# Kernel tuning notes

Measured on AMD Instinct MI355X. Metric: run time of the kernel, lower is better.

## Reference

```python
import jax, jax.numpy as jnp
import numpy as np

B, T = 32, 2048            # batch, seq_len
V = 16                     # vocab_size
H = 256                    # hidden_size
NV = V + 2                 # embedding rows (padding_idx=0 + vocab + delimiter)
NO = V + 1                 # head output size


def setup_inputs() -> dict:
    key = jax.random.key(0)
    ks = jax.random.split(key, 8)
    s = 1.0 / np.sqrt(H).astype(np.float32)
    tokens = jax.random.randint(ks[0], (B, T), 0, NV)
    embed = jax.random.normal(ks[1], (NV, H), jnp.float32) * 0.02
    embed = embed.at[0].set(0.0)  # padding_idx=0
    # GRU params (PyTorch layout: gates [r|z|n] stacked on last dim)
    W_ih = jax.random.uniform(ks[2], (H, 3 * H), jnp.float32, -s, s)
    W_hh = jax.random.uniform(ks[3], (H, 3 * H), jnp.float32, -s, s)
    b_ih = jax.random.uniform(ks[4], (3 * H,), jnp.float32, -s, s)
    b_hh = jax.random.uniform(ks[5], (3 * H,), jnp.float32, -s, s)
    W_head = jax.random.uniform(ks[6], (H, NO), jnp.float32, -s, s)
    b_head = jax.random.uniform(ks[7], (NO,), jnp.float32, -s, s)
    return {"tokens": tokens, "embed": embed, "W_ih": W_ih, "W_hh": W_hh,
            "b_ih": b_ih, "b_hh": b_hh, "W_head": W_head, "b_head": b_head}


def _mogru_scan(x, W_ih, W_hh, b_ih, b_hh):
    # x: [B, T, H]. Precompute all input projections in one big GEMM.
    gi = x @ W_ih + b_ih                      # [B, T, 3H]
    gi_t = jnp.swapaxes(gi, 0, 1)             # [T, B, 3H] for scan
    h0 = jnp.zeros((x.shape[0], W_hh.shape[0]), x.dtype)

    def step(h, gi_step):
        gh = h @ W_hh + b_hh                  # [B, 3H]
        i_r, i_z, i_n = jnp.split(gi_step, 3, axis=-1)
        h_r, h_z, h_n = jnp.split(gh, 3, axis=-1)
        r = jax.nn.sigmoid(i_r + h_r)
        z = jax.nn.sigmoid(i_z + h_z)         # beta: retention gate
        n = jnp.tanh(i_n + r * h_n)
        h_new = (1.0 - z) * n + z * h
        return h_new, (h_new, z)

    h_last, (outs, betas) = jax.lax.scan(step, h0, gi_t)
    return jnp.swapaxes(outs, 0, 1), h_last, jnp.swapaxes(betas, 0, 1)


def reference(tokens, embed, W_ih, W_hh, b_ih, b_hh, W_head, b_head):
    x = embed[tokens]                          # [B, T, H] embedding lookup
    output, _, betas = _mogru_scan(x, W_ih, W_hh, b_ih, b_hh)
    logits = output @ W_head + b_head          # [B, T, V+1]
    return logits, betas
```

## Files before the change

kernel.cpp:

```cpp
#include <hip/hip_runtime.h>

#define BB   32
#define TT   2048
#define HH   256
#define G3   768
#define NVOC 18
#define NOUT 17
#define LOGITS_ELEMS ((size_t)BB * TT * NOUT)

typedef _Float16 h2 __attribute__((ext_vector_type(2)));

__device__ __forceinline__ float bf1(unsigned short u){
  union{unsigned int i; float f;} v; v.i = ((unsigned int)u) << 16; return v.f;
}
__device__ __forceinline__ unsigned short f2bf(float f){
  union{float f; unsigned int i;} v; v.f = f;
  unsigned int lsb = (v.i >> 16) & 1u;
  v.i += 0x7fffu + lsb;
  return (unsigned short)(v.i >> 16);
}
__device__ __forceinline__ float bflo(unsigned int u){
  union{unsigned int i; float f;} v; v.i = u << 16; return v.f;
}
__device__ __forceinline__ float bfhi(unsigned int u){
  union{unsigned int i; float f;} v; v.i = u & 0xffff0000u; return v.f;
}

__device__ __forceinline__ float ld1(const float* p, size_t i){ return p[i]; }
__device__ __forceinline__ float ld1(const unsigned short* p, size_t i){ return bf1(p[i]); }

__device__ __forceinline__ bool detect_f32(const void* W_ih_raw){
  const unsigned short* u = (const unsigned short*)W_ih_raw;
  bool big = false;
  #pragma unroll
  for (int i = 0; i < 64; i++){
    float v = bf1(u[i]);
    big |= !(v >= -0.25f && v <= 0.25f);
  }
  return big;
}

#if __has_builtin(__builtin_amdgcn_fdot2)
#define FDOT2(a,b,c) __builtin_amdgcn_fdot2((a),(b),(c),false)
#else
#define FDOT2(a,b,c) ((c) + (float)(a).x*(float)(b).x + (float)(a).y*(float)(b).y)
#endif

template<typename T>
__device__ __forceinline__ void prep_body(const T* W_hh, _Float16* Wp){
  int j = blockIdx.x;
  int e = threadIdx.x;
  int q = j & 1, p = j >> 1;
  int c = e >> 7, i = e & 127;
  float v = ld1(W_hh, (size_t)(128*q + i) * G3 + 2*p + c);
  Wp[(size_t)j * 256 + e] = (_Float16)v;
}

__global__ __launch_bounds__(256) void k_prep(
    const void* __restrict__ W_hh, const void* __restrict__ W_ih,
    _Float16* __restrict__ Wp)
{
  if (detect_f32(W_ih)) prep_body<float>((const float*)W_hh, Wp);
  else                  prep_body<unsigned short>((const unsigned short*)W_hh, Wp);
}

template<typename T>
__device__ __forceinline__ void proj_body(const T* embed, const T* W_ih,
                                          const T* b_ih, const T* b_hh,
                                          float* proj, float* bb){
  __shared__ float s_e[HH];
  int v = blockIdx.x, j = threadIdx.x;
  if (j < HH) s_e[j] = ld1(embed, (size_t)v * HH + j);
  if (v == 0) bb[j] = ld1(b_hh, (size_t)j);
  __syncthreads();
  float acc = ld1(b_ih, (size_t)j);
  #pragma unroll 8
  for (int k = 0; k < HH; k++)
    acc += s_e[k] * ld1(W_ih, (size_t)k * G3 + j);
  proj[(size_t)v * G3 + j] = acc;
}

__global__ __launch_bounds__(768) void k_proj(
    const void* __restrict__ embed, const void* __restrict__ W_ih,
    const void* __restrict__ b_ih, const void* __restrict__ b_hh,
    float* __restrict__ proj, float* __restrict__ bb)
{
  if (detect_f32(W_ih))
    proj_body<float>((const float*)embed, (const float*)W_ih,
                     (const float*)b_ih, (const float*)b_hh, proj, bb);
  else
    proj_body<unsigned short>((const unsigned short*)embed,
                              (const unsigned short*)W_ih,
                              (const unsigned short*)b_ih,
                              (const unsigned short*)b_hh, proj, bb);
}

__global__ __launch_bounds__(768, 1) void k_scan(
    const int*      __restrict__ tokens,
    const _Float16* __restrict__ Wp,
    const float*    __restrict__ bb,
    const void*     __restrict__ W_ih,
    const float*    __restrict__ proj,
    unsigned short* __restrict__ outs,
    void*           __restrict__ d_out_base)
{
  __shared__ float s_proj[NVOC * G3];
  __shared__ __align__(16) h2 s_h[HH / 2];
  __shared__ float s_z[HH];
  __shared__ float s_n[HH];

  const bool f32m = detect_f32(W_ih);
  const int b = blockIdx.x;
  const int j = threadIdx.x;
  const int q16 = (j & 1) * 16;

  for (int i = j; i < NVOC * G3; i += 768) s_proj[i] = proj[i];

  h2 wA[64], wB[64];
  {
    const float4* wp4 = (const float4*)(Wp + (size_t)j * 256);
    #pragma unroll
    for (int i = 0; i < 16; i++){
      float4 v = wp4[i];
      wA[4*i+0] = __builtin_bit_cast(h2, v.x);
      wA[4*i+1] = __builtin_bit_cast(h2, v.y);
      wA[4*i+2] = __builtin_bit_cast(h2, v.z);
      wA[4*i+3] = __builtin_bit_cast(h2, v.w);
    }
    #pragma unroll
    for (int i = 0; i < 16; i++){
      float4 v = wp4[16 + i];
      wB[4*i+0] = __builtin_bit_cast(h2, v.x);
      wB[4*i+1] = __builtin_bit_cast(h2, v.y);
      wB[4*i+2] = __builtin_bit_cast(h2, v.z);
      wB[4*i+3] = __builtin_bit_cast(h2, v.w);
    }
  }
  const float bhh = bb[j];

  if (j < HH/2) { h2 z; z.x = (_Float16)0.f; z.y = (_Float16)0.f; s_h[j] = z; }
  float h_old = 0.f;

  const int* tptr = tokens + (size_t)b * TT;
  int tok = tptr[0];
  unsigned short* orow   = outs + (size_t)b * TT * HH + j;
  unsigned short* brow_b = (unsigned short*)d_out_base + LOGITS_ELEMS
                           + (size_t)b * TT * HH + (j - HH);
  float*          brow_f = (float*)d_out_base + LOGITS_ELEMS
                           + (size_t)b * TT * HH + (j - HH);

  __syncthreads();

  for (int t = 0; t < TT; t++) {
    int tok_next = (t + 1 < TT) ? tptr[t + 1] : 0;
    const float* pj = s_proj + tok * G3;
    float gi  = pj[j];
    float gin = (j < HH) ? pj[2*HH + j] : 0.f;

    float a0 = 0.f, a1 = 0.f, a2 = 0.f, a3 = 0.f;
    const int4* hp = (const int4*)s_h;
    #pragma unroll
    for (int i = 0; i < 16; i++) {
      int4 hv = hp[q16 + i];
      h2 x0 = __builtin_bit_cast(h2, hv.x);
      h2 x1 = __builtin_bit_cast(h2, hv.y);
      h2 x2 = __builtin_bit_cast(h2, hv.z);
      h2 x3 = __builtin_bit_cast(h2, hv.w);
      a0 = FDOT2(wA[4*i+0], x0, a0);
      a1 = FDOT2(wA[4*i+1], x1, a1);
      a0 = FDOT2(wA[4*i+2], x2, a0);
      a1 = FDOT2(wA[4*i+3], x3, a1);
      a2 = FDOT2(wB[4*i+0], x0, a2);
      a3 = FDOT2(wB[4*i+1], x1, a3);
      a2 = FDOT2(wB[4*i+2], x2, a2);
      a3 = FDOT2(wB[4*i+3], x3, a3);
    }
    float accA = a0 + a1;
    float accB = a2 + a3;
    accA += __shfl_xor(accA, 1);
    accB += __shfl_xor(accB, 1);
    float gh = ((j & 1) ? accB : accA) + bhh;

    float r = 0.f;
    if (j >= 2*HH) {
      s_n[j - 2*HH] = gh;
    } else if (j >= HH) {
      float z = 1.f / (1.f + __expf(-(gi + gh)));
      s_z[j - HH] = z;
      if (f32m) brow_f[(size_t)t * HH] = z;
      else      brow_b[(size_t)t * HH] = f2bf(z);
    } else {
      r = 1.f / (1.f + __expf(-(gi + gh)));
    }
    __syncthreads();

    if (j < HH) {
      float z = s_z[j];
      float x = gin + r * s_n[j];
      x = fminf(fmaxf(x, -15.f), 15.f);
      float e = __expf(2.f * x);
      float n = (e - 1.f) / (e + 1.f);
      float hn = (1.f - z) * n + z * h_old;
      h_old = hn;
      ((_Float16*)s_h)[j] = (_Float16)hn;
      orow[(size_t)t * HH] = f2bf(hn);
    }
    __syncthreads();
    tok = tok_next;
  }
}

template<typename T>
__device__ __forceinline__ void stage_head(const T* W_head, const T* b_head,
                                           float* s_w, float* s_b, int tid){
  for (int i = tid; i < NOUT * HH; i += 256) {
    int o = i / HH, k = i - o * HH;
    s_w[i] = ld1(W_head, (size_t)k * NOUT + o);
  }
  if (tid < NOUT) s_b[tid] = ld1(b_head, (size_t)tid);
}

__global__ __launch_bounds__(256) void k_head(
    const unsigned short* __restrict__ outs,
    const void* __restrict__ W_head,
    const void* __restrict__ b_head,
    const void* __restrict__ W_ih,
    void* __restrict__ logits_out)
{
  __shared__ float s_w[NOUT * HH];
  __shared__ float s_b[NOUT];
  const bool f32m = detect_f32(W_ih);
  const int tid = threadIdx.x;

  if (f32m) stage_head<float>((const float*)W_head, (const float*)b_head,
                              s_w, s_b, tid);
  else      stage_head<unsigned short>((const unsigned short*)W_head,
                                       (const unsigned short*)b_head,
                                       s_w, s_b, tid);
  __syncthreads();

  size_t gid = (size_t)blockIdx.x * 256 + tid;
  if (gid >= LOGITS_ELEMS) return;
  int o = (int)(gid % NOUT);
  size_t row = gid / NOUT;

  const uint4* xp = (const uint4*)(outs + row * HH);
  const float* wv = s_w + o * HH;
  float a0 = 0.f, a1 = 0.f, a2 = 0.f, a3 = 0.f;
  #pragma unroll 8
  for (int kk = 0; kk < 32; kk++) {
    uint4 u = xp[kk];
    int kb = kk * 8;
    a0 += bflo(u.x) * wv[kb+0] + bfhi(u.x) * wv[kb+1];
    a1 += bflo(u.y) * wv[kb+2] + bfhi(u.y) * wv[kb+3];
    a2 += bflo(u.z) * wv[kb+4] + bfhi(u.z) * wv[kb+5];
    a3 += bflo(u.w) * wv[kb+6] + bfhi(u.w) * wv[kb+7];
  }
  float val = ((a0 + a1) + (a2 + a3)) + s_b[o];
  if (f32m) ((float*)logits_out)[gid] = val;
  else      ((unsigned short*)logits_out)[gid] = f2bf(val);
}

extern "C" void kernel_launch(void* const* d_in, const int* in_sizes, int n_in,
                              void* d_out, int out_size, void* d_ws, size_t ws_size,
                              hipStream_t stream)
{
  const int* tokens = (const int*)d_in[0];
  const void* embed  = d_in[1];
  const void* W_ih   = d_in[2];
  const void* W_hh   = d_in[3];
  const void* b_ih   = d_in[4];
  const void* b_hh   = d_in[5];
  const void* W_head = d_in[6];
  const void* b_head = d_in[7];

  char* ws = (char*)d_ws;
  float*          proj = (float*)ws;
  float*          bb   = (float*)(ws + 55296);
  _Float16*       Wp   = (_Float16*)(ws + 55296 + 3072);
  unsigned short* outs = (unsigned short*)(ws + 55296 + 3072 + 393216);

  k_prep<<<G3, 256, 0, stream>>>(W_hh, W_ih, Wp);
  k_proj<<<NVOC, G3, 0, stream>>>(embed, W_ih, b_ih, b_hh, proj, bb);
  k_scan<<<BB, G3, 0, stream>>>(tokens, Wp, bb, W_ih, proj, outs, d_out);
  k_head<<<(int)((LOGITS_ELEMS + 255) / 256), 256, 0, stream>>>(
      outs, W_head, b_head, W_ih, d_out);
}
```

Baseline: 2.719 ms.

## Use MFMA for the recurrent h·W_hh product in the GRU scan

Replaces the per-thread fdot2 dot products in the scan kernel with 16x16x32 f16 MFMA instructions. W_hh is repacked into MFMA B-operand layout and held in registers across 8 waves, and h is broadcast as the A operand. The block shrinks from 768 to 512 threads, gate pre-activations are written to shared memory, and the gate math is consolidated onto 256 threads. Only row 0 of each MFMA output is used, so most of the matrix work is wasted. The intent is to shorten the serial per-timestep latency of the recurrence.

After: 3.381 ms. 24.4% more time.

```diff
diff --git a/kernel.cpp b/kernel.cpp
--- a/kernel.cpp
+++ b/kernel.cpp
@@ -8,7 +8,8 @@
 #define NOUT 17
 #define LOGITS_ELEMS ((size_t)BB * TT * NOUT)
 
-typedef _Float16 h2 __attribute__((ext_vector_type(2)));
+typedef _Float16 f16x8 __attribute__((ext_vector_type(8)));
+typedef float    f32x4 __attribute__((ext_vector_type(4)));
 
 __device__ __forceinline__ float bf1(unsigned short u){
   union{unsigned int i; float f;} v; v.i = ((unsigned int)u) << 16; return v.f;
@@ -40,20 +41,19 @@
   return big;
 }
 
-#if __has_builtin(__builtin_amdgcn_fdot2)
-#define FDOT2(a,b,c) __builtin_amdgcn_fdot2((a),(b),(c),false)
-#else
-#define FDOT2(a,b,c) ((c) + (float)(a).x*(float)(b).x + (float)(a).y*(float)(b).y)
-#endif
-
 template<typename T>
 __device__ __forceinline__ void prep_body(const T* W_hh, _Float16* Wp){
-  int j = blockIdx.x;
-  int e = threadIdx.x;
-  int q = j & 1, p = j >> 1;
-  int c = e >> 7, i = e & 127;
-  float v = ld1(W_hh, (size_t)(128*q + i) * G3 + 2*p + c);
-  Wp[(size_t)j * 256 + e] = (_Float16)v;
+  int s  = blockIdx.x * 256 + threadIdx.x;
+  int l  = s & 63;
+  int k0 = (s >> 6) & 7;
+  int t2 = s >> 9;
+  int row0 = 32*k0 + 8*(l >> 4);
+  int col  = 16*t2 + (l & 15);
+  f16x8 v;
+  #pragma unroll
+  for (int i2 = 0; i2 < 8; i2++)
+    v[i2] = (_Float16)ld1(W_hh, (size_t)(row0 + i2) * G3 + col);
+  ((f16x8*)Wp)[s] = v;
 }
 
 __global__ __launch_bounds__(256) void k_prep(
@@ -95,7 +95,7 @@
                               (const unsigned short*)b_hh, proj, bb);
 }
 
-__global__ __launch_bounds__(768, 1) void k_scan(
+__global__ __launch_bounds__(512, 2) void k_scan(
     const int*      __restrict__ tokens,
     const _Float16* __restrict__ Wp,
     const float*    __restrict__ bb,
@@ -105,108 +105,101 @@
     void*           __restrict__ d_out_base)
 {
   __shared__ float s_proj[NVOC * G3];
-  __shared__ __align__(16) h2 s_h[HH / 2];
-  __shared__ float s_z[HH];
-  __shared__ float s_n[HH];
+  __shared__ __align__(16) _Float16 s_h[HH];
+  __shared__ float s_gh[G3];
 
   const bool f32m = detect_f32(W_ih);
   const int b = blockIdx.x;
   const int j = threadIdx.x;
-  const int q16 = (j & 1) * 16;
-
-  for (int i = j; i < NVOC * G3; i += 768) s_proj[i] = proj[i];
-
-  h2 wA[64], wB[64];
+  const int w = j >> 6;
+  const int l = j & 63;
+  const int g = l >> 4;
+  const int c = l & 15;
+
+  for (int i = j; i < NVOC * G3 / 4; i += 512)
+    ((float4*)s_proj)[i] = ((const float4*)proj)[i];
+
+  f16x8 wB[48];
   {
-    const float4* wp4 = (const float4*)(Wp + (size_t)j * 256);
+    const f16x8* wpp = (const f16x8*)Wp + (size_t)w * 48 * 64 + l;
     #pragma unroll
-    for (int i = 0; i < 16; i++){
-      float4 v = wp4[i];
-      wA[4*i+0] = __builtin_bit_cast(h2, v.x);
-      wA[4*i+1] = __builtin_bit_cast(h2, v.y);
-      wA[4*i+2] = __builtin_bit_cast(h2, v.z);
-      wA[4*i+3] = __builtin_bit_cast(h2, v.w);
-    }
-    #pragma unroll
-    for (int i = 0; i < 16; i++){
-      float4 v = wp4[16 + i];
-      wB[4*i+0] = __builtin_bit_cast(h2, v.x);
-      wB[4*i+1] = __builtin_bit_cast(h2, v.y);
-      wB[4*i+2] = __builtin_bit_cast(h2, v.z);
-      wB[4*i+3] = __builtin_bit_cast(h2, v.w);
-    }
-  }
-  const float bhh = bb[j];
-
-  if (j < HH/2) { h2 z; z.x = (_Float16)0.f; z.y = (_Float16)0.f; s_h[j] = z; }
+    for (int i = 0; i < 48; i++) wB[i] = wpp[(size_t)i * 64];
+  }
+  const float bh0 = bb[96*w +  0 + c];
+  const float bh1 = bb[96*w + 16 + c];
+  const float bh2 = bb[96*w + 32 + c];
+  const float bh3 = bb[96*w + 48 + c];
+  const float bh4 = bb[96*w + 64 + c];
+  const float bh5 = bb[96*w + 80 + c];
+
+  if (j < HH) s_h[j] = (_Float16)0.f;
+
   float h_old = 0.f;
-
   const int* tptr = tokens + (size_t)b * TT;
-  int tok = tptr[0];
+  int tok = 0;
   unsigned short* orow   = outs + (size_t)b * TT * HH + j;
   unsigned short* brow_b = (unsigned short*)d_out_base + LOGITS_ELEMS
-                           + (size_t)b * TT * HH + (j - HH);
+                           + (size_t)b * TT * HH + j;
   float*          brow_f = (float*)d_out_base + LOGITS_ELEMS
-                           + (size_t)b * TT * HH + (j - HH);
+                           + (size_t)b * TT * HH + j;
+  if (j < HH) tok = tptr[0];
 
   __syncthreads();
 
+  const f16x8* hp8 = (const f16x8*)s_h;
+
   for (int t = 0; t < TT; t++) {
-    int tok_next = (t + 1 < TT) ? tptr[t + 1] : 0;
-    const float* pj = s_proj + tok * G3;
-    float gi  = pj[j];
-    float gin = (j < HH) ? pj[2*HH + j] : 0.f;
-
-    float a0 = 0.f, a1 = 0.f, a2 = 0.f, a3 = 0.f;
-    const int4* hp = (const int4*)s_h;
+    int tok_next = 0;
+    if (j < HH) tok_next = (t + 1 < TT) ? tptr[t + 1] : 0;
+
+    f32x4 acc0 = {bh0, bh0, bh0, bh0};
+    f32x4 acc1 = {bh1, bh1, bh1, bh1};
+    f32x4 acc2 = {bh2, bh2, bh2, bh2};
+    f32x4 acc3 = {bh3, bh3, bh3, bh3};
+    f32x4 acc4 = {bh4, bh4, bh4, bh4};
+    f32x4 acc5 = {bh5, bh5, bh5, bh5};
+
     #pragma unroll
-    for (int i = 0; i < 16; i++) {
-      int4 hv = hp[q16 + i];
-      h2 x0 = __builtin_bit_cast(h2, hv.x);
-      h2 x1 = __builtin_bit_cast(h2, hv.y);
-      h2 x2 = __builtin_bit_cast(h2, hv.z);
-      h2 x3 = __builtin_bit_cast(h2, hv.w);
-      a0 = FDOT2(wA[4*i+0], x0, a0);
-      a1 = FDOT2(wA[4*i+1], x1, a1);
-      a0 = FDOT2(wA[4*i+2], x2, a0);
-      a1 = FDOT2(wA[4*i+3], x3, a1);
-      a2 = FDOT2(wB[4*i+0], x0, a2);
-      a3 = FDOT2(wB[4*i+1], x1, a3);
-      a2 = FDOT2(wB[4*i+2], x2, a2);
-      a3 = FDOT2(wB[4*i+3], x3, a3);
+    for (int k0 = 0; k0 < 8; k0++) {
+      f16x8 af = hp8[4*k0 + g];
+      acc0 = __builtin_amdgcn_mfma_f32_16x16x32_f16(af, wB[ 0 + k0], acc0, 0, 0, 0);
+      acc1 = __builtin_amdgcn_mfma_f32_16x16x32_f16(af, wB[ 8 + k0], acc1, 0, 0, 0);
+      acc2 = __builtin_amdgcn_mfma_f32_16x16x32_f16(af, wB[16 + k0], acc2, 0, 0, 0);
+      acc3 = __builtin_amdgcn_mfma_f32_16x16x32_f16(af, wB[24 + k0], acc3, 0, 0, 0);
+      acc4 = __builtin_amdgcn_mfma_f32_16x16x32_f16(af, wB[32 + k0], acc4, 0, 0, 0);
+      acc5 = __builtin_amdgcn_mfma_f32_16x16x32_f16(af, wB[40 + k0], acc5, 0, 0, 0);
     }
-    float accA = a0 + a1;
-    float accB = a2 + a3;
-    accA += __shfl_xor(accA, 1);
-    accB += __shfl_xor(accB, 1);
-    float gh = ((j & 1) ? accB : accA) + bhh;
-
-    float r = 0.f;
-    if (j >= 2*HH) {
-      s_n[j - 2*HH] = gh;
-    } else if (j >= HH) {
-      float z = 1.f / (1.f + __expf(-(gi + gh)));
-      s_z[j - HH] = z;
+    {
+      float v1 = (g == 0) ? acc0[0] : (g == 1) ? acc1[0]
+               : (g == 2) ? acc2[0] : acc3[0];
+      s_gh[96*w + l] = v1;
+      if (l < 32) {
+        float v2 = (g == 0) ? acc4[0] : acc5[0];
+        s_gh[96*w + 64 + l] = v2;
+      }
+    }
+    __syncthreads();
+
+    if (j < HH) {
+      const float* pj = s_proj + tok * G3;
+      float ghr = s_gh[j];
+      float ghz = s_gh[HH + j];
+      float ghn = s_gh[2*HH + j];
+      float r = 1.f / (1.f + __expf(-(pj[j] + ghr)));
+      float z = 1.f / (1.f + __expf(-(pj[HH + j] + ghz)));
       if (f32m) brow_f[(size_t)t * HH] = z;
       else      brow_b[(size_t)t * HH] = f2bf(z);
-    } else {
-      r = 1.f / (1.f + __expf(-(gi + gh)));
-    }
-    __syncthreads();
-
-    if (j < HH) {
-      float z = s_z[j];
-      float x = gin + r * s_n[j];
+      float x = pj[2*HH + j] + r * ghn;
       x = fminf(fmaxf(x, -15.f), 15.f);
       float e = __expf(2.f * x);
       float n = (e - 1.f) / (e + 1.f);
       float hn = (1.f - z) * n + z * h_old;
       h_old = hn;
-      ((_Float16*)s_h)[j] = (_Float16)hn;
+      s_h[j] = (_Float16)hn;
       orow[(size_t)t * HH] = f2bf(hn);
+      tok = tok_next;
     }
     __syncthreads();
-    tok = tok_next;
   }
 }
 
@@ -280,9 +273,9 @@
   _Float16*       Wp   = (_Float16*)(ws + 55296 + 3072);
   unsigned short* outs = (unsigned short*)(ws + 55296 + 3072 + 393216);
 
-  k_prep<<<G3, 256, 0, stream>>>(W_hh, W_ih, Wp);
+  k_prep<<<96, 256, 0, stream>>>(W_hh, W_ih, Wp);
   k_proj<<<NVOC, G3, 0, stream>>>(embed, W_ih, b_ih, b_hh, proj, bb);
-  k_scan<<<BB, G3, 0, stream>>>(tokens, Wp, bb, W_ih, proj, outs, d_out);
+  k_scan<<<BB, 512, 0, stream>>>(tokens, Wp, bb, W_ih, proj, outs, d_out);
   k_head<<<(int)((LOGITS_ELEMS + 255) / 256), 256, 0, stream>>>(
       outs, W_head, b_head, W_ih, d_out);
 }
```

## Remap GRU scan to 512 threads computing all gates per hidden unit, one barrier per step

Applied to the files above, without the earlier changes.

The recurrent scan now uses 512 threads, where each pair of threads owns one hidden unit and computes its r, z and n gate dot products together. The gate combination then happens in registers after a DPP pair swap, so the s_z/s_n staging and one of the two per-step barriers are no longer needed. The hidden state is double-buffered in LDS and tokens are staged in shared memory. The intermediate output becomes fp16 so the head kernel can use fdot2 against fp16 weights. The cost is higher register pressure (48 float4 weight registers per thread) and a hand-written barrier asm.

Result: faster. 2.651 ms (-2.5%).

```diff
diff --git a/kernel.cpp b/kernel.cpp
--- a/kernel.cpp
+++ b/kernel.cpp
@@ -19,12 +19,6 @@
   v.i += 0x7fffu + lsb;
   return (unsigned short)(v.i >> 16);
 }
-__device__ __forceinline__ float bflo(unsigned int u){
-  union{unsigned int i; float f;} v; v.i = u << 16; return v.f;
-}
-__device__ __forceinline__ float bfhi(unsigned int u){
-  union{unsigned int i; float f;} v; v.i = u & 0xffff0000u; return v.f;
-}
 
 __device__ __forceinline__ float ld1(const float* p, size_t i){ return p[i]; }
 __device__ __forceinline__ float ld1(const unsigned short* p, size_t i){ return bf1(p[i]); }
@@ -46,22 +40,48 @@
 #define FDOT2(a,b,c) ((c) + (float)(a).x*(float)(b).x + (float)(a).y*(float)(b).y)
 #endif
 
+__device__ __forceinline__ h2 bch2(unsigned int u){ return __builtin_bit_cast(h2, u); }
+__device__ __forceinline__ h2 bch2f(float f){ return __builtin_bit_cast(h2, f); }
+
+__device__ __forceinline__ float pair_swap(float v){
+  int i = __builtin_bit_cast(int, v);
+  i = __builtin_amdgcn_mov_dpp(i, 0xB1, 0xF, 0xF, true);
+  return __builtin_bit_cast(float, i);
+}
+
+__device__ __forceinline__ void bar_lds(){
+  asm volatile("s_waitcnt lgkmcnt(0)\n\ts_barrier" ::: "memory");
+}
+
 template<typename T>
-__device__ __forceinline__ void prep_body(const T* W_hh, _Float16* Wp){
-  int j = blockIdx.x;
-  int e = threadIdx.x;
-  int q = j & 1, p = j >> 1;
-  int c = e >> 7, i = e & 127;
-  float v = ld1(W_hh, (size_t)(128*q + i) * G3 + 2*p + c);
-  Wp[(size_t)j * 256 + e] = (_Float16)v;
+__device__ __forceinline__ void prep_body(const T* W_hh, float4* Wp4){
+  int s   = blockIdx.x * 256 + threadIdx.x;
+  int tid = s & 511;
+  int jg  = s >> 9;
+  int p   = tid >> 1, q = tid & 1;
+  int g   = jg >> 4,  jx = jg & 15;
+  int col = (g << 8) + p;
+  int k0  = (q << 7) + (jx << 3);
+  float c0, c1, c2, c3;
+  #pragma unroll
+  for (int c = 0; c < 4; c++){
+    h2 pr;
+    pr.x = (_Float16)ld1(W_hh, (size_t)(k0 + 2*c    ) * G3 + col);
+    pr.y = (_Float16)ld1(W_hh, (size_t)(k0 + 2*c + 1) * G3 + col);
+    float fc = __builtin_bit_cast(float, pr);
+    if (c == 0) c0 = fc; else if (c == 1) c1 = fc;
+    else if (c == 2) c2 = fc; else c3 = fc;
+  }
+  float4 v; v.x = c0; v.y = c1; v.z = c2; v.w = c3;
+  Wp4[s] = v;
 }
 
 __global__ __launch_bounds__(256) void k_prep(
     const void* __restrict__ W_hh, const void* __restrict__ W_ih,
-    _Float16* __restrict__ Wp)
-{
-  if (detect_f32(W_ih)) prep_body<float>((const float*)W_hh, Wp);
-  else                  prep_body<unsigned short>((const unsigned short*)W_hh, Wp);
+    float4* __restrict__ Wp4)
+{
+  if (detect_f32(W_ih)) prep_body<float>((const float*)W_hh, Wp4);
+  else                  prep_body<unsigned short>((const unsigned short*)W_hh, Wp4);
 }
 
 template<typename T>
@@ -95,139 +115,136 @@
                               (const unsigned short*)b_hh, proj, bb);
 }
 
-__global__ __launch_bounds__(768, 1) void k_scan(
-    const int*      __restrict__ tokens,
-    const _Float16* __restrict__ Wp,
-    const float*    __restrict__ bb,
-    const void*     __restrict__ W_ih,
-    const float*    __restrict__ proj,
-    unsigned short* __restrict__ outs,
-    void*           __restrict__ d_out_base)
+__global__ __launch_bounds__(512, 2) void k_scan(
+    const int*    __restrict__ tokens,
+    const float4* __restrict__ Wp4,
+    const float*  __restrict__ bb,
+    const void*   __restrict__ W_ih,
+    const float*  __restrict__ proj,
+    _Float16*     __restrict__ outs,
+    void*         __restrict__ d_out_base)
 {
   __shared__ float s_proj[NVOC * G3];
-  __shared__ __align__(16) h2 s_h[HH / 2];
-  __shared__ float s_z[HH];
-  __shared__ float s_n[HH];
+  __shared__ int   s_tok[TT];
+  __shared__ __align__(16) _Float16 s_h[2][HH];
 
   const bool f32m = detect_f32(W_ih);
-  const int b = blockIdx.x;
-  const int j = threadIdx.x;
-  const int q16 = (j & 1) * 16;
-
-  for (int i = j; i < NVOC * G3; i += 768) s_proj[i] = proj[i];
-
-  h2 wA[64], wB[64];
+  const int b   = blockIdx.x;
+  const int tid = threadIdx.x;
+  const int p   = tid >> 1;
+  const int q   = tid & 1;
+
+  for (int i = tid; i < NVOC * G3 / 4; i += 512)
+    ((float4*)s_proj)[i] = ((const float4*)proj)[i];
+  ((int4*)s_tok)[tid] = ((const int4*)(tokens + (size_t)b * TT))[tid];
+
+  float4 wreg[48];
   {
-    const float4* wp4 = (const float4*)(Wp + (size_t)j * 256);
+    const float4* wp = Wp4 + tid;
     #pragma unroll
-    for (int i = 0; i < 16; i++){
-      float4 v = wp4[i];
-      wA[4*i+0] = __builtin_bit_cast(h2, v.x);
-      wA[4*i+1] = __builtin_bit_cast(h2, v.y);
-      wA[4*i+2] = __builtin_bit_cast(h2, v.z);
-      wA[4*i+3] = __builtin_bit_cast(h2, v.w);
+    for (int i = 0; i < 48; i++) wreg[i] = wp[(size_t)i * 512];
+  }
+  const float bhr = bb[p];
+  const float bhz = bb[HH + p];
+  const float bhn = bb[2*HH + p];
+
+  if (tid < HH) s_h[0][tid] = (_Float16)0.f;
+  float h_old = 0.f;
+
+  _Float16*       orow   = outs + (size_t)b * TT * HH + p;
+  unsigned short* brow_b = (unsigned short*)d_out_base + LOGITS_ELEMS
+                           + (size_t)b * TT * HH + p;
+  float*          brow_f = (float*)d_out_base + LOGITS_ELEMS
+                           + (size_t)b * TT * HH + p;
+
+  __syncthreads();
+
+  for (int t = 0; t < TT; t++) {
+    int tok = s_tok[t];
+    const float* pj = s_proj + tok * G3;
+    float gir = pj[p];
+    float giz = pj[HH + p];
+    float gin = pj[2*HH + p];
+
+    const int4* hb = (const int4*)(&s_h[t & 1][0]) + (q << 4);
+
+    float r0=0.f,r1=0.f,r2=0.f,r3=0.f;
+    float z0=0.f,z1=0.f,z2=0.f,z3=0.f;
+    float n0=0.f,n1=0.f,n2=0.f,n3=0.f;
+    #pragma unroll
+    for (int jx = 0; jx < 16; jx++) {
+      int4 hv = hb[jx];
+      h2 x0 = bch2((unsigned)hv.x);
+      h2 x1 = bch2((unsigned)hv.y);
+      h2 x2 = bch2((unsigned)hv.z);
+      h2 x3 = bch2((unsigned)hv.w);
+      float4 wr = wreg[jx];
+      float4 wz = wreg[16 + jx];
+      float4 wn = wreg[32 + jx];
+      r0 = FDOT2(bch2f(wr.x), x0, r0);
+      r1 = FDOT2(bch2f(wr.y), x1, r1);
+      r2 = FDOT2(bch2f(wr.z), x2, r2);
+      r3 = FDOT2(bch2f(wr.w), x3, r3);
+      z0 = FDOT2(bch2f(wz.x), x0, z0);
+      z1 = FDOT2(bch2f(wz.y), x1, z1);
+      z2 = FDOT2(bch2f(wz.z), x2, z2);
+      z3 = FDOT2(bch2f(wz.w), x3, z3);
+      n0 = FDOT2(bch2f(wn.x), x0, n0);
+      n1 = FDOT2(bch2f(wn.y), x1, n1);
+      n2 = FDOT2(bch2f(wn.z), x2, n2);
+      n3 = FDOT2(bch2f(wn.w), x3, n3);
     }
-    #pragma unroll
-    for (int i = 0; i < 16; i++){
-      float4 v = wp4[16 + i];
-      wB[4*i+0] = __builtin_bit_cast(h2, v.x);
-      wB[4*i+1] = __builtin_bit_cast(h2, v.y);
-      wB[4*i+2] = __builtin_bit_cast(h2, v.z);
-      wB[4*i+3] = __builtin_bit_cast(h2, v.w);
-    }
-  }
-  const float bhh = bb[j];
-
-  if (j < HH/2) { h2 z; z.x = (_Float16)0.f; z.y = (_Float16)0.f; s_h[j] = z; }
-  float h_old = 0.f;
-
-  const int* tptr = tokens + (size_t)b * TT;
-  int tok = tptr[0];
-  unsigned short* orow   = outs + (size_t)b * TT * HH + j;
-  unsigned short* brow_b = (unsigned short*)d_out_base + LOGITS_ELEMS
-                           + (size_t)b * TT * HH + (j - HH);
-  float*          brow_f = (float*)d_out_base + LOGITS_ELEMS
-                           + (size_t)b * TT * HH + (j - HH);
-
-  __syncthreads();
-
-  for (int t = 0; t < TT; t++) {
-    int tok_next = (t + 1 < TT) ? tptr[t + 1] : 0;
-    const float* pj = s_proj + tok * G3;
-    float gi  = pj[j];
-    float gin = (j < HH) ? pj[2*HH + j] : 0.f;
-
-    float a0 = 0.f, a1 = 0.f, a2 = 0.f, a3 = 0.f;
-    const int4* hp = (const int4*)s_h;
-    #pragma unroll
-    for (int i = 0; i < 16; i++) {
-      int4 hv = hp[q16 + i];
-      h2 x0 = __builtin_bit_cast(h2, hv.x);
-      h2 x1 = __builtin_bit_cast(h2, hv.y);
-      h2 x2 = __builtin_bit_cast(h2, hv.z);
-      h2 x3 = __builtin_bit_cast(h2, hv.w);
-      a0 = FDOT2(wA[4*i+0], x0, a0);
-      a1 = FDOT2(wA[4*i+1], x1, a1);
-      a0 = FDOT2(wA[4*i+2], x2, a0);
-      a1 = FDOT2(wA[4*i+3], x3, a1);
-      a2 = FDOT2(wB[4*i+0], x0, a2);
-      a3 = FDOT2(wB[4*i+1], x1, a3);
-      a2 = FDOT2(wB[4*i+2], x2, a2);
-      a3 = FDOT2(wB[4*i+3], x3, a3);
-    }
-    float accA = a0 + a1;
-    float accB = a2 + a3;
-    accA += __shfl_xor(accA, 1);
-    accB += __shfl_xor(accB, 1);
-    float gh = ((j & 1) ? accB : accA) + bhh;
-
-    float r = 0.f;
-    if (j >= 2*HH) {
-      s_n[j - 2*HH] = gh;
-    } else if (j >= HH) {
-      float z = 1.f / (1.f + __expf(-(gi + gh)));
-      s_z[j - HH] = z;
+    float ghr = (r0 + r1) + (r2 + r3);
+    float ghz = (z0 + z1) + (z2 + z3);
+    float ghn = (n0 + n1) + (n2 + n3);
+    ghr += pair_swap(ghr);
+    ghz += pair_swap(ghz);
+    ghn += pair_swap(ghn);
+    ghr += bhr; ghz += bhz; ghn += bhn;
+
+    float r = 1.f / (1.f + __expf(-(gir + ghr)));
+    float z = 1.f / (1.f + __expf(-(giz + ghz)));
+    float x = gin + r * ghn;
+    x = fminf(fmaxf(x, -15.f), 15.f);
+    float e = __expf(2.f * x);
+    float n = (e - 1.f) / (e + 1.f);
+    float hn = (1.f - z) * n + z * h_old;
+    h_old = hn;
+
+    if (q == 0) {
+      s_h[(t + 1) & 1][p] = (_Float16)hn;
+      orow[(size_t)t * HH] = (_Float16)hn;
+    } else {
       if (f32m) brow_f[(size_t)t * HH] = z;
       else      brow_b[(size_t)t * HH] = f2bf(z);
-    } else {
-      r = 1.f / (1.f + __expf(-(gi + gh)));
     }
-    __syncthreads();
-
-    if (j < HH) {
-      float z = s_z[j];
-      float x = gin + r * s_n[j];
-      x = fminf(fmaxf(x, -15.f), 15.f);
-      float e = __expf(2.f * x);
-      float n = (e - 1.f) / (e + 1.f);
-      float hn = (1.f - z) * n + z * h_old;
-      h_old = hn;
-      ((_Float16*)s_h)[j] = (_Float16)hn;
-      orow[(size_t)t * HH] = f2bf(hn);
-    }
-    __syncthreads();
-    tok = tok_next;
-  }
-}
+    bar_lds();
+  }
+}
+
+#define WSTR 129
 
 template<typename T>
 __device__ __forceinline__ void stage_head(const T* W_head, const T* b_head,
-                                           float* s_w, float* s_b, int tid){
-  for (int i = tid; i < NOUT * HH; i += 256) {
-    int o = i / HH, k = i - o * HH;
-    s_w[i] = ld1(W_head, (size_t)k * NOUT + o);
+                                           h2* s_w, float* s_b, int tid){
+  for (int i = tid; i < NOUT * 128; i += 256) {
+    int o = i >> 7, ip = i & 127;
+    h2 pr;
+    pr.x = (_Float16)ld1(W_head, (size_t)(2*ip    ) * NOUT + o);
+    pr.y = (_Float16)ld1(W_head, (size_t)(2*ip + 1) * NOUT + o);
+    s_w[o * WSTR + ip] = pr;
   }
   if (tid < NOUT) s_b[tid] = ld1(b_head, (size_t)tid);
 }
 
 __global__ __launch_bounds__(256) void k_head(
-    const unsigned short* __restrict__ outs,
+    const _Float16* __restrict__ outs,
     const void* __restrict__ W_head,
     const void* __restrict__ b_head,
     const void* __restrict__ W_ih,
     void* __restrict__ logits_out)
 {
-  __shared__ float s_w[NOUT * HH];
+  __shared__ h2 s_w[NOUT * WSTR];
   __shared__ float s_b[NOUT];
   const bool f32m = detect_f32(W_ih);
   const int tid = threadIdx.x;
@@ -245,16 +262,16 @@
   size_t row = gid / NOUT;
 
   const uint4* xp = (const uint4*)(outs + row * HH);
-  const float* wv = s_w + o * HH;
+  const h2* wv = s_w + o * WSTR;
   float a0 = 0.f, a1 = 0.f, a2 = 0.f, a3 = 0.f;
   #pragma unroll 8
   for (int kk = 0; kk < 32; kk++) {
     uint4 u = xp[kk];
-    int kb = kk * 8;
-    a0 += bflo(u.x) * wv[kb+0] + bfhi(u.x) * wv[kb+1];
-    a1 += bflo(u.y) * wv[kb+2] + bfhi(u.y) * wv[kb+3];
-    a2 += bflo(u.z) * wv[kb+4] + bfhi(u.z) * wv[kb+5];
-    a3 += bflo(u.w) * wv[kb+6] + bfhi(u.w) * wv[kb+7];
+    int kb = kk * 4;
+    a0 = FDOT2(bch2(u.x), wv[kb+0], a0);
+    a1 = FDOT2(bch2(u.y), wv[kb+1], a1);
+    a2 = FDOT2(bch2(u.z), wv[kb+2], a2);
+    a3 = FDOT2(bch2(u.w), wv[kb+3], a3);
   }
   float val = ((a0 + a1) + (a2 + a3)) + s_b[o];
   if (f32m) ((float*)logits_out)[gid] = val;
@@ -275,14 +292,14 @@
   const void* b_head = d_in[7];
 
   char* ws = (char*)d_ws;
-  float*          proj = (float*)ws;
-  float*          bb   = (float*)(ws + 55296);
-  _Float16*       Wp   = (_Float16*)(ws + 55296 + 3072);
-  unsigned short* outs = (unsigned short*)(ws + 55296 + 3072 + 393216);
-
-  k_prep<<<G3, 256, 0, stream>>>(W_hh, W_ih, Wp);
+  float*    proj = (float*)ws;
+  float*    bb   = (float*)(ws + 55296);
+  float4*   Wp4  = (float4*)(ws + 55296 + 3072);
+  _Float16* outs = (_Float16*)(ws + 55296 + 3072 + 393216);
+
+  k_prep<<<96, 256, 0, stream>>>(W_hh, W_ih, Wp4);
   k_proj<<<NVOC, G3, 0, stream>>>(embed, W_ih, b_ih, b_hh, proj, bb);
-  k_scan<<<BB, G3, 0, stream>>>(tokens, Wp, bb, W_ih, proj, outs, d_out);
+  k_scan<<<BB, 512, 0, stream>>>(tokens, Wp4, bb, W_ih, proj, outs, d_out);
   k_head<<<(int)((LOGITS_ELEMS + 255) / 256), 256, 0, stream>>>(
       outs, W_head, b_head, W_ih, d_out);
 }
```
